# Kernel optimization log

Measured on AMD Instinct MI355X. Metric: run time of the kernel, lower is better.

The kernel has to match this reference:

```python
import jax, jax.numpy as jnp
import numpy as np

D = 1152      # hidden_size
H = 16        # num_heads
K = D // H    # head_dim = 72
L = 2         # depth
I = 4304      # intermediate_size
M = 2         # spatial_merge_size
NPOS = 2304   # num_position_embeddings (48x48)
OUT = 2048    # out_hidden_size
CIN = 3 * 2 * 16 * 16  # C*tp*p*p = 1536
GRID = np.array([[1, 48, 48], [1, 32, 64], [2, 24, 40]], dtype=np.int32)


def _ln(x, s, b, eps=1e-6):
    mu = jnp.mean(x, -1, keepdims=True)
    var = jnp.mean((x - mu) ** 2, -1, keepdims=True)
    return (x - mu) * jax.lax.rsqrt(var + eps) * s + b


def _rot_half(x):
    h = x.shape[-1] // 2
    return jnp.concatenate([-x[..., h:], x[..., :h]], -1)


def _seg_bounds(g):
    b = [0]
    for t, h, w in g:
        for _ in range(int(t)):
            b.append(b[-1] + int(h) * int(w))
    return list(zip(b[:-1], b[1:]))


def _rope_cos_sin(g):
    half = K // 2  # rotary_half_dim
    max_hw = int(g[:, 1:].max())
    inv = 1.0 / (10000.0 ** (np.arange(0, half, 2, dtype=np.float64) / half))
    table = np.arange(max_hw)[:, None] * inv[None, :]  # (max_hw, half//2)
    pos = []
    for t, h, w in g:
        t, h, w = int(t), int(h), int(w)
        mh, mw = h // M, w // M
        row = np.broadcast_to(np.arange(mh)[:, None, None, None] * M + np.arange(M)[None, None, :, None], (mh, mw, M, M)).reshape(-1)
        col = np.broadcast_to(np.arange(mw)[None, :, None, None] * M + np.arange(M)[None, None, None, :], (mh, mw, M, M)).reshape(-1)
        c = np.stack([row, col], -1)
        if t > 1:
            c = np.tile(c, (t, 1))
        pos.append(c)
    pos = np.concatenate(pos, 0)
    emb = table[pos].reshape(pos.shape[0], -1)     # (N, half)
    emb = np.concatenate([emb, emb], -1)           # (N, head_dim)
    return jnp.asarray(np.cos(emb), jnp.float32), jnp.asarray(np.sin(emb), jnp.float32)


def _pos_embeds(pos_table, g):
    n = int(NPOS ** 0.5)
    outs = []
    for t, h, w in g:
        t, h, w = int(t), int(h), int(w)
        hi = np.linspace(0, n - 1, h); wi = np.linspace(0, n - 1, w)
        hf = np.floor(hi).astype(np.int32); wf = np.floor(wi).astype(np.int32)
        hc = np.clip(hf + 1, 0, n - 1); wc = np.clip(wf + 1, 0, n - 1)
        dh = (hi - hf).astype(np.float32); dw = (wi - wf).astype(np.float32)
        i00 = (hf[:, None] * n + wf[None, :]).reshape(-1)
        i01 = (hf[:, None] * n + wc[None, :]).reshape(-1)
        i10 = (hc[:, None] * n + wf[None, :]).reshape(-1)
        i11 = (hc[:, None] * n + wc[None, :]).reshape(-1)
        w00 = ((1 - dh)[:, None] * (1 - dw)[None, :]).reshape(-1, 1)
        w01 = ((1 - dh)[:, None] * dw[None, :]).reshape(-1, 1)
        w10 = (dh[:, None] * (1 - dw)[None, :]).reshape(-1, 1)
        w11 = (dh[:, None] * dw[None, :]).reshape(-1, 1)
        e = pos_table[i00] * w00 + pos_table[i01] * w01 + pos_table[i10] * w10 + pos_table[i11] * w11
        # spatial-merge reorder
        e = jnp.tile(e, (t, 1)).reshape(t, h // M, M, w // M, M, -1).transpose(0, 1, 3, 2, 4, 5).reshape(-1, D)
        outs.append(e)
    return jnp.concatenate(outs, 0)


def _forward(pixel_values, grid, patch_w, patch_b, pos_table, ln1_s, ln1_b, qkv_w, qkv_b,
             proj_w, proj_b, ln2_s, ln2_b, fc1_w, fc1_b, fc2_w, fc2_b,
             m_ln_s, m_ln_b, m_fc1_w, m_fc1_b, m_fc2_w, m_fc2_b):
    g = np.asarray(grid)
    # patch embed: conv with kernel==stride over whole patch == matmul on flattened patch
    x = pixel_values @ patch_w + patch_b               # (N, D)
    x = x + _pos_embeds(pos_table, g)
    cos, sin = _rope_cos_sin(g)                        # (N, K) each
    bounds = _seg_bounds(g)
    scale = K ** -0.5
    for l in range(L):
        h = _ln(x, ln1_s[l], ln1_b[l])
        N = h.shape[0]
        qkv = (h @ qkv_w[l] + qkv_b[l]).reshape(N, 3, H, K)
        q, k, v = qkv[:, 0], qkv[:, 1], qkv[:, 2]
        q = q * cos[:, None, :] + _rot_half(q) * sin[:, None, :]
        k = k * cos[:, None, :] + _rot_half(k) * sin[:, None, :]
        outs = []
        for s, e in bounds:  # static ragged segments (cu_seqlens)
            logits = jnp.einsum('lhk,mhk->hlm', q[s:e], k[s:e]) * scale
            wts = jax.nn.softmax(logits.astype(jnp.float32), -1).astype(logits.dtype)
            outs.append(jnp.einsum('hlm,mhk->lhk', wts, v[s:e]).reshape(e - s, H * K))
        attn = jnp.concatenate(outs, 0) @ proj_w[l] + proj_b[l]
        x = x + attn
        h2 = _ln(x, ln2_s[l], ln2_b[l])
        x = x + jax.nn.gelu(h2 @ fc1_w[l] + fc1_b[l], approximate=True) @ fc2_w[l] + fc2_b[l]
    normed = _ln(x, m_ln_s, m_ln_b).reshape(-1, D * M * M)
    return jax.nn.gelu(normed @ m_fc1_w + m_fc1_b, approximate=True) @ m_fc2_w + m_fc2_b


def setup_inputs() -> dict:
    key = jax.random.key(0)
    ks = jax.random.split(key, 16)
    def nrm(k, shp, s=0.02):
        return jax.random.normal(k, shp, jnp.float32) * s
    Ntok = int(sum(int(t) * int(h) * int(w) for t, h, w in GRID))  # 6272
    return {
        'pixel_values': nrm(ks[0], (Ntok, CIN), 1.0),
        'grid_thw': jnp.asarray(GRID),
        'patch_w': nrm(ks[1], (CIN, D)), 'patch_b': nrm(ks[2], (D,), 0.01),
        'pos_table': nrm(ks[3], (NPOS, D)),
        'ln1_s': jnp.ones((L, D)), 'ln1_b': jnp.zeros((L, D)),
        'qkv_w': nrm(ks[4], (L, D, 3 * D)), 'qkv_b': nrm(ks[5], (L, 3 * D), 0.01),
        'proj_w': nrm(ks[6], (L, D, D)), 'proj_b': nrm(ks[7], (L, D), 0.01),
        'ln2_s': jnp.ones((L, D)), 'ln2_b': jnp.zeros((L, D)),
        'fc1_w': nrm(ks[8], (L, D, I)), 'fc1_b': nrm(ks[9], (L, I), 0.01),
        'fc2_w': nrm(ks[10], (L, I, D)), 'fc2_b': nrm(ks[11], (L, D), 0.01),
        'm_ln_s': jnp.ones((D,)), 'm_ln_b': jnp.zeros((D,)),
        'm_fc1_w': nrm(ks[12], (D * M * M, D * M * M)), 'm_fc1_b': nrm(ks[13], (D * M * M,), 0.01),
        'm_fc2_w': nrm(ks[14], (D * M * M, OUT)), 'm_fc2_b': nrm(ks[15], (OUT,), 0.01),
    }


def reference(pixel_values, grid_thw, patch_w, patch_b, pos_table, ln1_s, ln1_b, qkv_w, qkv_b,
              proj_w, proj_b, ln2_s, ln2_b, fc1_w, fc1_b, fc2_w, fc2_b,
              m_ln_s, m_ln_b, m_fc1_w, m_fc1_b, m_fc2_w, m_fc2_b):
    return _forward(pixel_values, grid_thw, patch_w, patch_b, pos_table, ln1_s, ln1_b, qkv_w, qkv_b,
                    proj_w, proj_b, ln2_s, ln2_b, fc1_w, fc1_b, fc2_w, fc2_b,
                    m_ln_s, m_ln_b, m_fc1_w, m_fc1_b, m_fc2_w, m_fc2_b)
```

## Files before the change

### kernel.cpp

```cpp
#include <hip/hip_runtime.h>

typedef __bf16 bf16;
typedef float f32x4 __attribute__((ext_vector_type(4)));
typedef bf16 bf16x8 __attribute__((ext_vector_type(8)));

#define NTOK 6272
#define DMODEL 1152

__device__ __forceinline__ void tok_geo(int t, int& row, int& col, int& gh, int& gw) {
    int local;
    if (t < 2304)      { local = t;        gh = 48; gw = 48; }
    else if (t < 4352) { local = t - 2304; gh = 32; gw = 64; }
    else if (t < 5312) { local = t - 4352; gh = 24; gw = 40; }
    else               { local = t - 5312; gh = 24; gw = 40; }
    int mc = local & 1;
    int mr = (local >> 1) & 1;
    int rest = local >> 2;
    int mwc = gw >> 1;
    int mw = rest % mwc;
    int mh = rest / mwc;
    row = mh * 2 + mr;
    col = mw * 2 + mc;
}

__device__ __forceinline__ float gelu_tanh(float v) {
    float c = v + 0.044715f * v * v * v;
    return 0.5f * v * (1.0f + tanhf(0.7978845608028654f * c));
}

__global__ void detect_kernel(const unsigned short* __restrict__ px, int* __restrict__ flag) {
    int tid = threadIdx.x;
    int cnt = 0;
    for (int i = tid * 8; i < tid * 8 + 8; i++) {
        unsigned e = (px[i] >> 7) & 0xFF;
        if (e < 100u || e > 140u) cnt++;
    }
#pragma unroll
    for (int off = 32; off > 0; off >>= 1) cnt += __shfl_down(cnt, off);
    if (tid == 0) *flag = (cnt > 64) ? 1 : 0;
}

template <typename T>
__device__ __forceinline__ void load8(const T* src, bf16* dst, bool pred) {
    if (!pred) {
        uint4 z = {0, 0, 0, 0};
        *(uint4*)dst = z;
        return;
    }
    if constexpr (sizeof(T) == 2) {
        *(uint4*)dst = *(const uint4*)src;
    } else {
        float4 a = *(const float4*)src;
        float4 b = *(const float4*)(src + 4);
        dst[0] = (bf16)a.x; dst[1] = (bf16)a.y; dst[2] = (bf16)a.z; dst[3] = (bf16)a.w;
        dst[4] = (bf16)b.x; dst[5] = (bf16)b.y; dst[6] = (bf16)b.z; dst[7] = (bf16)b.w;
    }
}

template <typename TI>
__global__ __launch_bounds__(256) void pos_embed_kernel(const int* __restrict__ flag,
                                                        const TI* __restrict__ tab,
                                                        bf16* __restrict__ x) {
    if (*flag != (sizeof(TI) == 4 ? 1 : 0)) return;
    int t = blockIdx.x;
    int row, col, gh, gw;
    tok_geo(t, row, col, gh, gw);
    float hi = row * 47.0f / (gh - 1);
    float wi = col * 47.0f / (gw - 1);
    int hf = (int)hi, wf = (int)wi;
    int hc = min(hf + 1, 47), wc = min(wf + 1, 47);
    float dh = hi - hf, dw = wi - wf;
    float w00 = (1.f - dh) * (1.f - dw);
    float w01 = (1.f - dh) * dw;
    float w10 = dh * (1.f - dw);
    float w11 = dh * dw;
    const TI* p00 = tab + (size_t)(hf * 48 + wf) * DMODEL;
    const TI* p01 = tab + (size_t)(hf * 48 + wc) * DMODEL;
    const TI* p10 = tab + (size_t)(hc * 48 + wf) * DMODEL;
    const TI* p11 = tab + (size_t)(hc * 48 + wc) * DMODEL;
    bf16* xr = x + (size_t)t * DMODEL;
    for (int d = threadIdx.x; d < DMODEL; d += 256)
        xr[d] = (bf16)(w00 * (float)p00[d] + w01 * (float)p01[d] +
                       w10 * (float)p10[d] + w11 * (float)p11[d]);
}

template <typename TI>
__global__ __launch_bounds__(256) void ln_kernel(const int* __restrict__ flag,
                                                 const bf16* __restrict__ x,
                                                 const TI* __restrict__ s,
                                                 const TI* __restrict__ b,
                                                 bf16* __restrict__ out) {
    if (*flag != (sizeof(TI) == 4 ? 1 : 0)) return;
    const int row = blockIdx.x;
    const int tid = threadIdx.x;
    __shared__ float red[4];
    const bf16* xr = x + (size_t)row * DMODEL;
    float vals[5];
    int cnt = 0;
    float sum = 0.f;
    for (int i = tid; i < DMODEL; i += 256) { vals[cnt] = (float)xr[i]; sum += vals[cnt]; cnt++; }
#pragma unroll
    for (int off = 32; off > 0; off >>= 1) sum += __shfl_down(sum, off);
    if ((tid & 63) == 0) red[tid >> 6] = sum;
    __syncthreads();
    float mean = (red[0] + red[1] + red[2] + red[3]) * (1.0f / DMODEL);
    float vs = 0.f;
    for (int i = 0; i < cnt; i++) { float d = vals[i] - mean; vs += d * d; }
#pragma unroll
    for (int off = 32; off > 0; off >>= 1) vs += __shfl_down(vs, off);
    __syncthreads();
    if ((tid & 63) == 0) red[tid >> 6] = vs;
    __syncthreads();
    float var = (red[0] + red[1] + red[2] + red[3]) * (1.0f / DMODEL);
    float inv = rsqrtf(var + 1e-6f);
    int idx = 0;
    for (int i = tid; i < DMODEL; i += 256)
        out[(size_t)row * DMODEL + i] = (bf16)((vals[idx++] - mean) * inv * (float)s[i] + (float)b[i]);
}

__global__ __launch_bounds__(256) void rope_inplace_kernel(bf16* __restrict__ qkv) {
    int idx = blockIdx.x * 256 + threadIdx.x;
    const int total = NTOK * 16 * 36;
    if (idx >= total) return;
    int j = idx % 36;
    int rest = idx / 36;
    int h = rest & 15;
    int t = rest >> 4;
    bf16* base = qkv + (size_t)t * 3456 + h * 72;
    int row, col, gh, gw;
    tok_geo(t, row, col, gh, gw);
    float pos = (float)((j < 18) ? row : col);
    int fi = (j < 18) ? j : j - 18;
    float ang = pos * powf(10000.0f, -(float)fi / 18.0f);
    float cv = cosf(ang), sv = sinf(ang);
    float q0v = (float)base[j],        q1v = (float)base[j + 36];
    float k0v = (float)base[1152 + j], k1v = (float)base[1152 + j + 36];
    base[j]          = (bf16)(q0v * cv - q1v * sv);
    base[j + 36]     = (bf16)(q1v * cv + q0v * sv);
    base[1152 + j]      = (bf16)(k0v * cv - k1v * sv);
    base[1152 + j + 36] = (bf16)(k1v * cv + k0v * sv);
}

__global__ __launch_bounds__(256) void attn_kernel(const bf16* __restrict__ qkv,
                                                   bf16* __restrict__ outp) {
    const int bx = blockIdx.x;
    const int head = bx & 15;
    const int qt = bx >> 4;
    int sbase, slen, qtb;
    if (qt < 36)      { sbase = 0;    slen = 2304; qtb = 0;  }
    else if (qt < 68) { sbase = 2304; slen = 2048; qtb = 36; }
    else if (qt < 83) { sbase = 4352; slen = 960;  qtb = 68; }
    else              { sbase = 5312; slen = 960;  qtb = 83; }
    const int q0 = sbase + (qt - qtb) * 64;

    __shared__ bf16 Ks[64][104];
    __shared__ bf16 Vs[80][72];
    __shared__ bf16 Ps[64][72];

    const int tid = threadIdx.x;
    const int wv = tid >> 6;
    const int lane = tid & 63;
    const int quad = lane >> 4;
    const int l15 = lane & 15;

    const size_t hoff = (size_t)head * 72;

    for (int c = tid; c < 64; c += 256) {
        int r = 72 + (c >> 3), cc = (c & 7) * 8;
        uint4 z = {0, 0, 0, 0};
        *(uint4*)&Vs[r][cc] = z;
    }

    for (int c = tid; c < 768; c += 256) {
        int r = c / 12, cc = (c % 12) * 8;
        uint4 v = {0, 0, 0, 0};
        if (cc < 72) v = *(const uint4*)(qkv + (size_t)(q0 + r) * 3456 + hoff + cc);
        *(uint4*)&Ks[r][cc] = v;
    }
    __syncthreads();
    bf16x8 aq[3];
#pragma unroll
    for (int i = 0; i < 3; i++) aq[i] = *(const bf16x8*)&Ks[wv * 16 + l15][i * 32 + quad * 8];

    f32x4 o[5] = {};
    float m_i[4], l_i[4];
#pragma unroll
    for (int r = 0; r < 4; r++) { m_i[r] = -1e30f; l_i[r] = 0.f; }

    const float C1 = 0.17002234f;
    const int nkv = slen >> 6;
    for (int kt = 0; kt < nkv; kt++) {
        const int k0 = sbase + kt * 64;
        __syncthreads();
        for (int c = tid; c < 768; c += 256) {
            int r = c / 12, cc = (c % 12) * 8;
            uint4 v = {0, 0, 0, 0};
            if (cc < 72) v = *(const uint4*)(qkv + (size_t)(k0 + r) * 3456 + 1152 + hoff + cc);
            *(uint4*)&Ks[r][cc] = v;
        }
        for (int c = tid; c < 576; c += 256) {
            int r = c & 63, cc = (c >> 6) * 8;
            uint4 v = *(const uint4*)(qkv + (size_t)(k0 + r) * 3456 + 2304 + hoff + cc);
            const bf16* e = (const bf16*)&v;
#pragma unroll
            for (int i = 0; i < 8; i++) Vs[cc + i][r] = e[i];
        }
        __syncthreads();

        f32x4 sfr[4] = {};
#pragma unroll
        for (int kc = 0; kc < 3; kc++)
#pragma unroll
            for (int nt = 0; nt < 4; nt++) {
                bf16x8 bk = *(const bf16x8*)&Ks[nt * 16 + l15][kc * 32 + quad * 8];
                sfr[nt] = __builtin_amdgcn_mfma_f32_16x16x32_bf16(aq[kc], bk, sfr[nt], 0, 0, 0);
            }

        float mx[4];
#pragma unroll
        for (int reg = 0; reg < 4; reg++) {
            float m = fmaxf(fmaxf(sfr[0][reg], sfr[1][reg]), fmaxf(sfr[2][reg], sfr[3][reg]));
            m = fmaxf(m, __shfl_xor(m, 1));
            m = fmaxf(m, __shfl_xor(m, 2));
            m = fmaxf(m, __shfl_xor(m, 4));
            m = fmaxf(m, __shfl_xor(m, 8));
            mx[reg] = m;
        }
        bool grow = (mx[0] > m_i[0]) || (mx[1] > m_i[1]) || (mx[2] > m_i[2]) || (mx[3] > m_i[3]);
        if (__any(grow)) {
#pragma unroll
            for (int reg = 0; reg < 4; reg++) {
                float mn = fmaxf(m_i[reg], mx[reg]);
                float a = __builtin_amdgcn_exp2f((m_i[reg] - mn) * C1);
                m_i[reg] = mn;
                l_i[reg] *= a;
#pragma unroll
                for (int nt = 0; nt < 5; nt++) o[nt][reg] *= a;
            }
        }
        float mc[4];
#pragma unroll
        for (int reg = 0; reg < 4; reg++) mc[reg] = m_i[reg] * C1;
        float rs[4] = {0.f, 0.f, 0.f, 0.f};
#pragma unroll
        for (int nt = 0; nt < 4; nt++)
#pragma unroll
            for (int reg = 0; reg < 4; reg++) {
                float p = __builtin_amdgcn_exp2f(fmaf(sfr[nt][reg], C1, -mc[reg]));
                sfr[nt][reg] = p;
                rs[reg] += p;
            }
#pragma unroll
        for (int reg = 0; reg < 4; reg++) {
            float r = rs[reg];
            r += __shfl_xor(r, 1);
            r += __shfl_xor(r, 2);
            r += __shfl_xor(r, 4);
            r += __shfl_xor(r, 8);
            l_i[reg] += r;
        }

#pragma unroll
        for (int nt = 0; nt < 4; nt++)
#pragma unroll
            for (int reg = 0; reg < 4; reg++)
                Ps[wv * 16 + quad * 4 + reg][nt * 16 + l15] = (bf16)sfr[nt][reg];

#pragma unroll
        for (int kc = 0; kc < 2; kc++) {
            bf16x8 ap = *(const bf16x8*)&Ps[wv * 16 + l15][kc * 32 + quad * 8];
#pragma unroll
            for (int nt = 0; nt < 5; nt++) {
                bf16x8 bv = *(const bf16x8*)&Vs[nt * 16 + l15][kc * 32 + quad * 8];
                o[nt] = __builtin_amdgcn_mfma_f32_16x16x32_bf16(ap, bv, o[nt], 0, 0, 0);
            }
        }
    }

#pragma unroll
    for (int nt = 0; nt < 5; nt++)
#pragma unroll
        for (int reg = 0; reg < 4; reg++) {
            int c = nt * 16 + l15;
            if (c < 72) {
                int tok = q0 + wv * 16 + quad * 4 + reg;
                outp[(size_t)tok * DMODEL + head * 72 + c] = (bf16)(o[nt][reg] / l_i[reg]);
            }
        }
}

template <int MODE, typename TA, typename TB>
__global__ __launch_bounds__(256) void gemm_kernel(const int* __restrict__ flag,
                                                   const TA* __restrict__ A,
                                                   const TB* __restrict__ B,
                                                   const TB* __restrict__ bias,
                                                   void* __restrict__ outp,
                                                   int M, int N, int K) {
    if (*flag != (sizeof(TB) == 4 ? 1 : 0)) return;
    __shared__ bf16 As[128][40];
    __shared__ bf16 Bs[128][40];
    const int tid = threadIdx.x;
    const int m0 = blockIdx.y * 128;
    const int n0 = blockIdx.x * 128;
    const int wv = tid >> 6;
    const int lane = tid & 63;
    const int quad = lane >> 4;
    const int l15 = lane & 15;
    const int wr = (wv >> 1) * 64;
    const int wc = (wv & 1) * 64;

    const int a_row = tid >> 1;
    const int a_col = (tid & 1) * 16;
    const int b_k = tid & 31;
    const int b_n = (tid >> 5) * 16;

    f32x4 acc[4][4] = {};

    for (int k0 = 0; k0 < K; k0 += 32) {
        __syncthreads();
        {
            bf16 ea[16];
            int gr = m0 + a_row;
            const TA* ap = A + (size_t)gr * K + k0 + a_col;
// ... 23 lines not shown
#pragma unroll
            for (int ni = 0; ni < 4; ni++)
                acc[mi][ni] = __builtin_amdgcn_mfma_f32_16x16x32_bf16(af[mi], bfv[ni], acc[mi][ni], 0, 0, 0);
    }

#pragma unroll
    for (int mi = 0; mi < 4; mi++) {
#pragma unroll
        for (int ni = 0; ni < 4; ni++) {
#pragma unroll
            for (int reg = 0; reg < 4; reg++) {
                int r = m0 + wr + mi * 16 + quad * 4 + reg;
                int c = n0 + wc + ni * 16 + l15;
                if (r < M && c < N) {
                    float v = acc[mi][ni][reg] + (float)bias[c];
                    if (MODE == 1) v = gelu_tanh(v);
                    if (MODE == 2) {
                        bf16* o = (bf16*)outp;
                        size_t idx = (size_t)r * N + c;
                        o[idx] = (bf16)((float)o[idx] + v);
                    } else if (MODE == 3) {
                        TB* o = (TB*)outp;
                        o[(size_t)r * N + c] = (TB)v;
                    } else {
                        bf16* o = (bf16*)outp;
                        o[(size_t)r * N + c] = (bf16)v;
                    }
                }
            }
        }
    }
}


template <typename TI>
__global__ __launch_bounds__(256) void cvt_kernel(const int* __restrict__ flag,
                                                  const TI* __restrict__ in,
                                                  bf16* __restrict__ out, int n8) {
    if (*flag != (sizeof(TI) == 4 ? 1 : 0)) return;
    for (int i = blockIdx.x * 256 + threadIdx.x; i < n8; i += gridDim.x * 256) {
        bf16 e[8];
        load8(in + (size_t)i * 8, e, true);
        *(uint4*)(out + (size_t)i * 8) = *(uint4*)e;
    }
}

template <typename TI>
__global__ __launch_bounds__(256) void transpose_w_kernel(const int* __restrict__ flag,
                                                          const TI* __restrict__ B,
                                                          bf16* __restrict__ T,
                                                          int K, int N, int Kpad) {
    if (*flag != (sizeof(TI) == 4 ? 1 : 0)) return;
    __shared__ bf16 t[64][72];
    const int k0 = blockIdx.y * 64, n0 = blockIdx.x * 64;
    const int tid = threadIdx.x;
    const int kk = tid >> 2;
    const int nn0 = (tid & 3) * 16;
    bf16 e[16];
    bool ok = (k0 + kk < K) && (n0 + nn0 < N);
    const TI* src = B + (size_t)(k0 + kk) * N + n0 + nn0;
    load8(src, e, ok);
    load8(src + 8, e + 8, ok);
#pragma unroll
    for (int i = 0; i < 16; i++) t[nn0 + i][kk] = e[i];
    __syncthreads();
    const int nn = tid >> 2;
    const int j16 = (tid & 3) * 16;
    if (n0 + nn < N && k0 + j16 < Kpad) {
        bf16* dst = T + (size_t)(n0 + nn) * Kpad + k0 + j16;
        *(uint4*)dst = *(uint4*)&t[nn][j16];
        *(uint4*)(dst + 8) = *(uint4*)&t[nn][j16 + 8];
    }
}

template <typename TI>
__global__ __launch_bounds__(256) void cvt_bias_kernel(const int* __restrict__ flag,
        const TI* p0, const TI* p1, const TI* p2, const TI* p3, const TI* p4,
        const TI* p5, const TI* p6, const TI* p7, const TI* p8, const TI* p9,
        const TI* p10, bf16* __restrict__ out) {
    if (*flag != (sizeof(TI) == 4 ? 1 : 0)) return;
    const int lens[11] = {1152, 3456, 3456, 1152, 1152, 4304, 4304, 1152, 1152, 4608, 2048};
    const int offs[11] = {0, 1152, 4608, 8064, 9216, 10368, 14672, 18976, 20128, 21280, 25888};
    int b = blockIdx.x;
    const TI* src = (b == 0) ? p0 : (b == 1) ? p1 : (b == 2) ? p2 : (b == 3) ? p3
                  : (b == 4) ? p4 : (b == 5) ? p5 : (b == 6) ? p6 : (b == 7) ? p7
                  : (b == 8) ? p8 : (b == 9) ? p9 : p10;
    for (int i = threadIdx.x; i < lens[b]; i += 256) out[offs[b] + i] = (bf16)(float)src[i];
}

typedef const __attribute__((address_space(1))) void* gas_ptr;
typedef __attribute__((address_space(3))) void* las_ptr;
__device__ __forceinline__ void gload16(const bf16* g, bf16* l) {
    __builtin_amdgcn_global_load_lds((gas_ptr)g, (las_ptr)l, 16, 0, 0);
}

template <int MODE>
__global__ __launch_bounds__(256) void gemm_lds_kernel(const int* __restrict__ flag,
        const bf16* __restrict__ A, const bf16* __restrict__ BT,
        const bf16* __restrict__ bias, void* __restrict__ outp,
        int M, int N, int K, int ldc) {
    __shared__ bf16 As[128][32];
    __shared__ bf16 Bs[128][32];
    const int tid = threadIdx.x;
    const int m0 = blockIdx.y * 128;
    const int n0 = blockIdx.x * 128;
    const int wv = tid >> 6;
    const int lane = tid & 63;
    const int quad = lane >> 4;
    const int l15 = lane & 15;
    const int wr = (wv >> 1) * 64;
    const int wc = (wv & 1) * 64;

    const int sr = wv * 32 + (lane >> 2);
    const int sc = (lane & 3) * 8;
    const bf16* aP0 = A + (size_t)min(m0 + sr, M - 1) * K + sc;
    const bf16* aP1 = A + (size_t)min(m0 + sr + 16, M - 1) * K + sc;
    const bf16* bP0 = BT + (size_t)min(n0 + sr, N - 1) * K + sc;
    const bf16* bP1 = BT + (size_t)min(n0 + sr + 16, N - 1) * K + sc;
    bf16* lA0 = &As[wv * 32][0];
    bf16* lA1 = &As[wv * 32 + 16][0];
    bf16* lB0 = &Bs[wv * 32][0];
// ... 127 lines not shown
    }
}

#define OFF_PATCH  0ULL
#define OFF_QKV    1769472ULL
#define QKV_SZ     3981312ULL
#define OFF_PROJ   9732096ULL
#define PROJ_SZ    1327104ULL
#define OFF_FC1    12386304ULL
#define FC1_SZ     4958208ULL
#define OFF_FC2    22302720ULL
#define FC2_SZ     4976640ULL
#define OFF_MFC1   32256000ULL
#define OFF_MFC2   53489664ULL
#define OFF_BIAS   62926848ULL
#define WS_NEEDED  209001280ULL

extern "C" void kernel_launch(void* const* d_in, const int* in_sizes, int n_in,
                              void* d_out, int out_size, void* d_ws, size_t ws_size,
                              hipStream_t stream) {
    char* ws = (char*)d_ws;
    int* flag  = (int*)ws;
    bf16* x    = (bf16*)(ws + 256);
    bf16* h    = (bf16*)(ws + 256 + 14450688);
    bf16* bufA = (bf16*)(ws + 256 + 28901376);

    detect_kernel<<<1, 64, 0, stream>>>((const unsigned short*)d_in[0], flag);

    if (ws_size >= WS_NEEDED) {
        bf16* wT = (bf16*)(ws + 256 + 28901376 + 54190080);
        bf16* bias = wT + OFF_BIAS;
        bf16* px = bufA;

        cvt_kernel<bf16><<<1024, 256, 0, stream>>>(flag, (const bf16*)d_in[0], px, 1204224);
        cvt_kernel<float><<<1024, 256, 0, stream>>>(flag, (const float*)d_in[0], px, 1204224);

        auto T2 = [&](const void* srcBase, size_t eoff, bf16* dst, int K, int N, int Kpad) {
            dim3 g((N + 63) / 64, (Kpad + 63) / 64);
            transpose_w_kernel<bf16><<<g, 256, 0, stream>>>(flag, (const bf16*)srcBase + eoff, dst, K, N, Kpad);
            transpose_w_kernel<float><<<g, 256, 0, stream>>>(flag, (const float*)srcBase + eoff, dst, K, N, Kpad);
        };
        T2(d_in[2], 0, wT + OFF_PATCH, 1536, 1152, 1536);
        for (int l = 0; l < 2; l++) {
            T2(d_in[7],  (size_t)l * 1152 * 3456, wT + OFF_QKV + l * QKV_SZ, 1152, 3456, 1152);
            T2(d_in[9],  (size_t)l * 1152 * 1152, wT + OFF_PROJ + l * PROJ_SZ, 1152, 1152, 1152);
            T2(d_in[13], (size_t)l * 1152 * 4304, wT + OFF_FC1 + l * FC1_SZ, 1152, 4304, 1152);
            T2(d_in[15], (size_t)l * 4304 * 1152, wT + OFF_FC2 + l * FC2_SZ, 4304, 1152, 4320);
        }
        T2(d_in[19], 0, wT + OFF_MFC1, 4608, 4608, 4608);
        T2(d_in[21], 0, wT + OFF_MFC2, 4608, 2048, 4608);

        cvt_bias_kernel<bf16><<<11, 256, 0, stream>>>(flag,
            (const bf16*)d_in[3],
            (const bf16*)d_in[8], (const bf16*)d_in[8] + 3456,
            (const bf16*)d_in[10], (const bf16*)d_in[10] + 1152,
            (const bf16*)d_in[14], (const bf16*)d_in[14] + 4304,
            (const bf16*)d_in[16], (const bf16*)d_in[16] + 1152,
            (const bf16*)d_in[20], (const bf16*)d_in[22], bias);
        cvt_bias_kernel<float><<<11, 256, 0, stream>>>(flag,
            (const float*)d_in[3],
            (const float*)d_in[8], (const float*)d_in[8] + 3456,
            (const float*)d_in[10], (const float*)d_in[10] + 1152,
            (const float*)d_in[14], (const float*)d_in[14] + 4304,
            (const float*)d_in[16], (const float*)d_in[16] + 1152,
            (const float*)d_in[20], (const float*)d_in[22], bias);

        pos_embed_kernel<bf16><<<NTOK, 256, 0, stream>>>(flag, (const bf16*)d_in[4], x);
        pos_embed_kernel<float><<<NTOK, 256, 0, stream>>>(flag, (const float*)d_in[4], x);

        gemm_lds64_kernel<2><<<dim3(9, 98), 256, 0, stream>>>(flag, px, wT + OFF_PATCH,
                                                              bias + 0, x, NTOK, 1152, 1536, 1152);

        for (int l = 0; l < 2; l++) {
            ln_kernel<bf16><<<NTOK, 256, 0, stream>>>(flag, x, (const bf16*)d_in[5] + l * 1152,
                                                      (const bf16*)d_in[6] + l * 1152, h);
            ln_kernel<float><<<NTOK, 256, 0, stream>>>(flag, x, (const float*)d_in[5] + l * 1152,
                                                       (const float*)d_in[6] + l * 1152, h);
            gemm_lds_kernel<0><<<dim3(27, 49), 256, 0, stream>>>(flag, h, wT + OFF_QKV + l * QKV_SZ,
                                                                 bias + 1152 + l * 3456, bufA,
                                                                 NTOK, 3456, 1152, 3456);
            rope_inplace_kernel<<<(NTOK * 16 * 36 + 255) / 256, 256, 0, stream>>>(bufA);
            attn_kernel<<<98 * 16, 256, 0, stream>>>(bufA, h);
            gemm_lds64_kernel<2><<<dim3(9, 98), 256, 0, stream>>>(flag, h, wT + OFF_PROJ + l * PROJ_SZ,
                                                                  bias + 8064 + l * 1152, x,
                                                                  NTOK, 1152, 1152, 1152);
            ln_kernel<bf16><<<NTOK, 256, 0, stream>>>(flag, x, (const bf16*)d_in[11] + l * 1152,
                                                      (const bf16*)d_in[12] + l * 1152, h);
            ln_kernel<float><<<NTOK, 256, 0, stream>>>(flag, x, (const float*)d_in[11] + l * 1152,
                                                       (const float*)d_in[12] + l * 1152, h);
            gemm_lds_kernel<1><<<dim3(34, 49), 256, 0, stream>>>(flag, h, wT + OFF_FC1 + l * FC1_SZ,
                                                                 bias + 10368 + l * 4304, bufA,
                                                                 NTOK, 4304, 1152, 4320);
            gemm_lds64_kernel<2><<<dim3(9, 98), 256, 0, stream>>>(flag, bufA, wT + OFF_FC2 + l * FC2_SZ,
                                                                  bias + 18976 + l * 1152, x,
                                                                  NTOK, 1152, 4320, 1152);
        }
        ln_kernel<bf16><<<NTOK, 256, 0, stream>>>(flag, x, (const bf16*)d_in[17], (const bf16*)d_in[18], h);
        ln_kernel<float><<<NTOK, 256, 0, stream>>>(flag, x, (const float*)d_in[17], (const float*)d_in[18], h);
        gemm_lds_kernel<1><<<dim3(36, 13), 256, 0, stream>>>(flag, h, wT + OFF_MFC1,
                                                             bias + 21280, bufA, 1568, 4608, 4608, 4608);
        gemm_lds64_kernel<3><<<dim3(16, 25), 256, 0, stream>>>(flag, bufA, wT + OFF_MFC2,
                                                               bias + 25888, d_out, 1568, 2048, 4608, 2048);
        return;
    }

    {
        pos_embed_kernel<bf16><<<NTOK, 256, 0, stream>>>(flag, (const bf16*)d_in[4], x);
        pos_embed_kernel<float><<<NTOK, 256, 0, stream>>>(flag, (const float*)d_in[4], x);
        gemm_kernel<2, bf16, bf16><<<dim3(9, 49), 256, 0, stream>>>(
            flag, (const bf16*)d_in[0], (const bf16*)d_in[2], (const bf16*)d_in[3], x, NTOK, 1152, 1536);
        gemm_kernel<2, float, float><<<dim3(9, 49), 256, 0, stream>>>(
            flag, (const float*)d_in[0], (const float*)d_in[2], (const float*)d_in[3], x, NTOK, 1152, 1536);
    }
    for (int l = 0; l < 2; l++) {
        ln_kernel<bf16><<<NTOK, 256, 0, stream>>>(flag, x, (const bf16*)d_in[5] + l * 1152,
                                                  (const bf16*)d_in[6] + l * 1152, h);
        ln_kernel<float><<<NTOK, 256, 0, stream>>>(flag, x, (const float*)d_in[5] + l * 1152,
                                                   (const float*)d_in[6] + l * 1152, h);
        gemm_kernel<0, bf16, bf16><<<dim3(27, 49), 256, 0, stream>>>(
            flag, h, (const bf16*)d_in[7] + (size_t)l * 1152 * 3456,
            (const bf16*)d_in[8] + l * 3456, bufA, NTOK, 3456, 1152);
        gemm_kernel<0, bf16, float><<<dim3(27, 49), 256, 0, stream>>>(
            flag, h, (const float*)d_in[7] + (size_t)l * 1152 * 3456,
            (const float*)d_in[8] + l * 3456, bufA, NTOK, 3456, 1152);
        rope_inplace_kernel<<<(NTOK * 16 * 36 + 255) / 256, 256, 0, stream>>>(bufA);
        attn_kernel<<<98 * 16, 256, 0, stream>>>(bufA, h);
        gemm_kernel<2, bf16, bf16><<<dim3(9, 49), 256, 0, stream>>>(
            flag, h, (const bf16*)d_in[9] + (size_t)l * 1152 * 1152,
            (const bf16*)d_in[10] + l * 1152, x, NTOK, 1152, 1152);
        gemm_kernel<2, bf16, float><<<dim3(9, 49), 256, 0, stream>>>(
            flag, h, (const float*)d_in[9] + (size_t)l * 1152 * 1152,
            (const float*)d_in[10] + l * 1152, x, NTOK, 1152, 1152);
        ln_kernel<bf16><<<NTOK, 256, 0, stream>>>(flag, x, (const bf16*)d_in[11] + l * 1152,
// ... 28 lines not shown
```

Before: 2.212 ms.

## Merge dtype-templated kernel pairs, add MFMA setprio, use 64-row tile for merger fc1

```diff
diff --git a/kernel.cpp b/kernel.cpp
--- a/kernel.cpp
+++ b/kernel.cpp
@@ -55,6 +55,309 @@
         dst[0] = (bf16)a.x; dst[1] = (bf16)a.y; dst[2] = (bf16)a.z; dst[3] = (bf16)a.w;
         dst[4] = (bf16)b.x; dst[5] = (bf16)b.y; dst[6] = (bf16)b.z; dst[7] = (bf16)b.w;
     }
+}
+
+
+__global__ __launch_bounds__(256) void pos_embed2_kernel(const int* __restrict__ flag,
+                                                         const bf16* __restrict__ tab16,
+                                                         const float* __restrict__ tab32,
+                                                         bf16* __restrict__ x) {
+    const bool f32 = (*flag != 0);
+    int t = blockIdx.x;
+    int row, col, gh, gw;
+    tok_geo(t, row, col, gh, gw);
+    float hi = row * 47.0f / (gh - 1);
+    float wi = col * 47.0f / (gw - 1);
+    int hf = (int)hi, wf = (int)wi;
+    int hc = min(hf + 1, 47), wc = min(wf + 1, 47);
+    float dh = hi - hf, dw = wi - wf;
+    float w00 = (1.f - dh) * (1.f - dw);
+    float w01 = (1.f - dh) * dw;
+    float w10 = dh * (1.f - dw);
+    float w11 = dh * dw;
+    size_t i00 = (size_t)(hf * 48 + wf) * DMODEL;
+    size_t i01 = (size_t)(hf * 48 + wc) * DMODEL;
+    size_t i10 = (size_t)(hc * 48 + wf) * DMODEL;
+    size_t i11 = (size_t)(hc * 48 + wc) * DMODEL;
+    bf16* xr = x + (size_t)t * DMODEL;
+    if (f32) {
+        for (int d = threadIdx.x; d < DMODEL; d += 256)
+            xr[d] = (bf16)(w00 * tab32[i00 + d] + w01 * tab32[i01 + d] +
+                           w10 * tab32[i10 + d] + w11 * tab32[i11 + d]);
+    } else {
+        for (int d = threadIdx.x; d < DMODEL; d += 256)
+            xr[d] = (bf16)(w00 * (float)tab16[i00 + d] + w01 * (float)tab16[i01 + d] +
+                           w10 * (float)tab16[i10 + d] + w11 * (float)tab16[i11 + d]);
+    }
+}
+
+__global__ __launch_bounds__(256) void ln2_kernel(const int* __restrict__ flag,
+                                                  const bf16* __restrict__ x,
+                                                  const bf16* __restrict__ s16,
+                                                  const bf16* __restrict__ b16,
+                                                  const float* __restrict__ s32,
+                                                  const float* __restrict__ b32,
+                                                  bf16* __restrict__ out) {
+    const bool f32 = (*flag != 0);
+    const int row = blockIdx.x;
+    const int tid = threadIdx.x;
+    __shared__ float red[4];
+    const bf16* xr = x + (size_t)row * DMODEL;
+    float vals[5];
+    int cnt = 0;
+    float sum = 0.f;
+    for (int i = tid; i < DMODEL; i += 256) { vals[cnt] = (float)xr[i]; sum += vals[cnt]; cnt++; }
+#pragma unroll
+    for (int off = 32; off > 0; off >>= 1) sum += __shfl_down(sum, off);
+    if ((tid & 63) == 0) red[tid >> 6] = sum;
+    __syncthreads();
+    float mean = (red[0] + red[1] + red[2] + red[3]) * (1.0f / DMODEL);
+    float vs = 0.f;
+    for (int i = 0; i < cnt; i++) { float d = vals[i] - mean; vs += d * d; }
+#pragma unroll
+    for (int off = 32; off > 0; off >>= 1) vs += __shfl_down(vs, off);
+    __syncthreads();
+    if ((tid & 63) == 0) red[tid >> 6] = vs;
+    __syncthreads();
+    float var = (red[0] + red[1] + red[2] + red[3]) * (1.0f / DMODEL);
+    float inv = rsqrtf(var + 1e-6f);
+    int idx = 0;
+    for (int i = tid; i < DMODEL; i += 256) {
+        float sv = f32 ? s32[i] : (float)s16[i];
+        float bv = f32 ? b32[i] : (float)b16[i];
+        out[(size_t)row * DMODEL + i] = (bf16)((vals[idx++] - mean) * inv * sv + bv);
+    }
+}
+
+__global__ __launch_bounds__(256) void cvt2_kernel(const int* __restrict__ flag,
+                                                   const bf16* __restrict__ in16,
+                                                   const float* __restrict__ in32,
+                                                   bf16* __restrict__ out, int n8) {
+    const bool f32 = (*flag != 0);
+    for (int i = blockIdx.x * 256 + threadIdx.x; i < n8; i += gridDim.x * 256) {
+        bf16 e[8];
+        if (f32) load8(in32 + (size_t)i * 8, e, true);
+        else     load8(in16 + (size_t)i * 8, e, true);
+        *(uint4*)(out + (size_t)i * 8) = *(uint4*)e;
+    }
+}
+
+__global__ __launch_bounds__(256) void transpose_w2_kernel(const int* __restrict__ flag,
+                                                           const bf16* __restrict__ B16,
+                                                           const float* __restrict__ B32,
+                                                           bf16* __restrict__ T,
+                                                           int K, int N, int Kpad) {
+    const bool f32 = (*flag != 0);
+    __shared__ bf16 t[64][72];
+    const int k0 = blockIdx.y * 64, n0 = blockIdx.x * 64;
+    const int tid = threadIdx.x;
+    const int kk = tid >> 2;
+    const int nn0 = (tid & 3) * 16;
+    bf16 e[16];
+    bool ok = (k0 + kk < K) && (n0 + nn0 < N);
+    size_t idx = (size_t)(k0 + kk) * N + n0 + nn0;
+    if (f32) { load8(B32 + idx, e, ok); load8(B32 + idx + 8, e + 8, ok); }
+    else     { load8(B16 + idx, e, ok); load8(B16 + idx + 8, e + 8, ok); }
+#pragma unroll
+    for (int i = 0; i < 16; i++) t[nn0 + i][kk] = e[i];
+    __syncthreads();
+    const int nn = tid >> 2;
+    const int j16 = (tid & 3) * 16;
+    if (n0 + nn < N && k0 + j16 < Kpad) {
+        bf16* dst = T + (size_t)(n0 + nn) * Kpad + k0 + j16;
+        *(uint4*)dst = *(uint4*)&t[nn][j16];
+        *(uint4*)(dst + 8) = *(uint4*)&t[nn][j16 + 8];
+    }
+}
+
+template <typename TI>
+__global__ __launch_bounds__(256) void cvt_bias_kernel(const int* __restrict__ flag,
+        const TI* p0, const TI* p1, const TI* p2, const TI* p3, const TI* p4,
+        const TI* p5, const TI* p6, const TI* p7, const TI* p8, const TI* p9,
+        const TI* p10, bf16* __restrict__ out) {
+    if (*flag != (sizeof(TI) == 4 ? 1 : 0)) return;
+    const int lens[11] = {1152, 3456, 3456, 1152, 1152, 4304, 4304, 1152, 1152, 4608, 2048};
+    const int offs[11] = {0, 1152, 4608, 8064, 9216, 10368, 14672, 18976, 20128, 21280, 25888};
+    int b = blockIdx.x;
+    const TI* src = (b == 0) ? p0 : (b == 1) ? p1 : (b == 2) ? p2 : (b == 3) ? p3
+                  : (b == 4) ? p4 : (b == 5) ? p5 : (b == 6) ? p6 : (b == 7) ? p7
+                  : (b == 8) ? p8 : (b == 9) ? p9 : p10;
+    for (int i = threadIdx.x; i < lens[b]; i += 256) out[offs[b] + i] = (bf16)(float)src[i];
+}
+
+__global__ __launch_bounds__(256) void rope_inplace_kernel(bf16* __restrict__ qkv) {
+    int idx = blockIdx.x * 256 + threadIdx.x;
+    const int total = NTOK * 16 * 36;
+    if (idx >= total) return;
+    int j = idx % 36;
+    int rest = idx / 36;
+    int h = rest & 15;
+    int t = rest >> 4;
+    bf16* base = qkv + (size_t)t * 3456 + h * 72;
+    int row, col, gh, gw;
+    tok_geo(t, row, col, gh, gw);
+    float pos = (float)((j < 18) ? row : col);
+    int fi = (j < 18) ? j : j - 18;
+    float ang = pos * powf(10000.0f, -(float)fi / 18.0f);
+    float cv = cosf(ang), sv = sinf(ang);
+    float q0v = (float)base[j],        q1v = (float)base[j + 36];
+    float k0v = (float)base[1152 + j], k1v = (float)base[1152 + j + 36];
+    base[j]          = (bf16)(q0v * cv - q1v * sv);
+    base[j + 36]     = (bf16)(q1v * cv + q0v * sv);
+    base[1152 + j]      = (bf16)(k0v * cv - k1v * sv);
+    base[1152 + j + 36] = (bf16)(k1v * cv + k0v * sv);
+}
+
+__global__ __launch_bounds__(256) void attn_kernel(const bf16* __restrict__ qkv,
+                                                   bf16* __restrict__ outp) {
+    const int bx = blockIdx.x;
+    const int head = bx & 15;
+    const int qt = bx >> 4;
+    int sbase, slen, qtb;
+    if (qt < 36)      { sbase = 0;    slen = 2304; qtb = 0;  }
+    else if (qt < 68) { sbase = 2304; slen = 2048; qtb = 36; }
+    else if (qt < 83) { sbase = 4352; slen = 960;  qtb = 68; }
+    else              { sbase = 5312; slen = 960;  qtb = 83; }
+    const int q0 = sbase + (qt - qtb) * 64;
+
+    __shared__ bf16 Ks[64][104];
+    __shared__ bf16 Vs[80][72];
+    __shared__ bf16 Ps[64][72];
+
+    const int tid = threadIdx.x;
+    const int wv = tid >> 6;
+    const int lane = tid & 63;
+    const int quad = lane >> 4;
+    const int l15 = lane & 15;
+
+    const size_t hoff = (size_t)head * 72;
+
+    for (int c = tid; c < 64; c += 256) {
+        int r = 72 + (c >> 3), cc = (c & 7) * 8;
+        uint4 z = {0, 0, 0, 0};
+        *(uint4*)&Vs[r][cc] = z;
+    }
+
+    for (int c = tid; c < 768; c += 256) {
+        int r = c / 12, cc = (c % 12) * 8;
+        uint4 v = {0, 0, 0, 0};
+        if (cc < 72) v = *(const uint4*)(qkv + (size_t)(q0 + r) * 3456 + hoff + cc);
+        *(uint4*)&Ks[r][cc] = v;
+    }
+    __syncthreads();
+    bf16x8 aq[3];
+#pragma unroll
+    for (int i = 0; i < 3; i++) aq[i] = *(const bf16x8*)&Ks[wv * 16 + l15][i * 32 + quad * 8];
+
+    f32x4 o[5] = {};
+    float m_i[4], l_i[4];
+#pragma unroll
+    for (int r = 0; r < 4; r++) { m_i[r] = -1e30f; l_i[r] = 0.f; }
+
+    const float C1 = 0.17002234f;
+    const int nkv = slen >> 6;
+    for (int kt = 0; kt < nkv; kt++) {
+        const int k0 = sbase + kt * 64;
+        __syncthreads();
+        for (int c = tid; c < 768; c += 256) {
+            int r = c / 12, cc = (c % 12) * 8;
+            uint4 v = {0, 0, 0, 0};
+            if (cc < 72) v = *(const uint4*)(qkv + (size_t)(k0 + r) * 3456 + 1152 + hoff + cc);
+            *(uint4*)&Ks[r][cc] = v;
+        }
+        for (int c = tid; c < 576; c += 256) {
+            int r = c & 63, cc = (c >> 6) * 8;
+            uint4 v = *(const uint4*)(qkv + (size_t)(k0 + r) * 3456 + 2304 + hoff + cc);
+            const bf16* e = (const bf16*)&v;
+#pragma unroll
+            for (int i = 0; i < 8; i++) Vs[cc + i][r] = e[i];
+        }
+        __syncthreads();
+
+        f32x4 sfr[4] = {};
+        __builtin_amdgcn_s_setprio(1);
+#pragma unroll
+        for (int kc = 0; kc < 3; kc++)
+#pragma unroll
+            for (int nt = 0; nt < 4; nt++) {
+                bf16x8 bk = *(const bf16x8*)&Ks[nt * 16 + l15][kc * 32 + quad * 8];
+                sfr[nt] = __builtin_amdgcn_mfma_f32_16x16x32_bf16(aq[kc], bk, sfr[nt], 0, 0, 0);
+            }
+        __builtin_amdgcn_s_setprio(0);
+
+        float mx[4];
+#pragma unroll
+        for (int reg = 0; reg < 4; reg++) {
+            float m = fmaxf(fmaxf(sfr[0][reg], sfr[1][reg]), fmaxf(sfr[2][reg], sfr[3][reg]));
+            m = fmaxf(m, __shfl_xor(m, 1));
+            m = fmaxf(m, __shfl_xor(m, 2));
+            m = fmaxf(m, __shfl_xor(m, 4));
+            m = fmaxf(m, __shfl_xor(m, 8));
+            mx[reg] = m;
+        }
+        bool grow = (mx[0] > m_i[0]) || (mx[1] > m_i[1]) || (mx[2] > m_i[2]) || (mx[3] > m_i[3]);
+        if (__any(grow)) {
+#pragma unroll
+            for (int reg = 0; reg < 4; reg++) {
+                float mn = fmaxf(m_i[reg], mx[reg]);
+                float a = __builtin_amdgcn_exp2f((m_i[reg] - mn) * C1);
+                m_i[reg] = mn;
+                l_i[reg] *= a;
+#pragma unroll
+                for (int nt = 0; nt < 5; nt++) o[nt][reg] *= a;
+            }
+        }
+        float mc[4];
+#pragma unroll
+        for (int reg = 0; reg < 4; reg++) mc[reg] = m_i[reg] * C1;
+        float rs[4] = {0.f, 0.f, 0.f, 0.f};
+#pragma unroll
+        for (int nt = 0; nt < 4; nt++)
+#pragma unroll
+            for (int reg = 0; reg < 4; reg++) {
+                float p = __builtin_amdgcn_exp2f(fmaf(sfr[nt][reg], C1, -mc[reg]));
+                sfr[nt][reg] = p;
+                rs[reg] += p;
+            }
+#pragma unroll
+        for (int reg = 0; reg < 4; reg++) {
+            float r = rs[reg];
+            r += __shfl_xor(r, 1);
+            r += __shfl_xor(r, 2);
+            r += __shfl_xor(r, 4);
+            r += __shfl_xor(r, 8);
+            l_i[reg] += r;
+        }
+
+#pragma unroll
+        for (int nt = 0; nt < 4; nt++)
+#pragma unroll
+            for (int reg = 0; reg < 4; reg++)
+                Ps[wv * 16 + quad * 4 + reg][nt * 16 + l15] = (bf16)sfr[nt][reg];
+
+        __builtin_amdgcn_s_setprio(1);
+#pragma unroll
+        for (int kc = 0; kc < 2; kc++) {
+            bf16x8 ap = *(const bf16x8*)&Ps[wv * 16 + l15][kc * 32 + quad * 8];
+#pragma unroll
+            for (int nt = 0; nt < 5; nt++) {
+                bf16x8 bv = *(const bf16x8*)&Vs[nt * 16 + l15][kc * 32 + quad * 8];
+                o[nt] = __builtin_amdgcn_mfma_f32_16x16x32_bf16(ap, bv, o[nt], 0, 0, 0);
+            }
+        }
+        __builtin_amdgcn_s_setprio(0);
+    }
+
+#pragma unroll
+    for (int nt = 0; nt < 5; nt++)
+#pragma unroll
+        for (int reg = 0; reg < 4; reg++) {
+            int c = nt * 16 + l15;
+            if (c < 72) {
+                int tok = q0 + wv * 16 + quad * 4 + reg;
+                outp[(size_t)tok * DMODEL + head * 72 + c] = (bf16)(o[nt][reg] / l_i[reg]);
+            }
+        }
 }
 
 template <typename TI>
@@ -118,177 +421,6 @@
         out[(size_t)row * DMODEL + i] = (bf16)((vals[idx++] - mean) * inv * (float)s[i] + (float)b[i]);
 }
 
-__global__ __launch_bounds__(256) void rope_inplace_kernel(bf16* __restrict__ qkv) {
-    int idx = blockIdx.x * 256 + threadIdx.x;
-    const int total = NTOK * 16 * 36;
-    if (idx >= total) return;
-    int j = idx % 36;
-    int rest = idx / 36;
-    int h = rest & 15;
-    int t = rest >> 4;
-    bf16* base = qkv + (size_t)t * 3456 + h * 72;
-    int row, col, gh, gw;
-    tok_geo(t, row, col, gh, gw);
-    float pos = (float)((j < 18) ? row : col);
-    int fi = (j < 18) ? j : j - 18;
-    float ang = pos * powf(10000.0f, -(float)fi / 18.0f);
-    float cv = cosf(ang), sv = sinf(ang);
-    float q0v = (float)base[j],        q1v = (float)base[j + 36];
-    float k0v = (float)base[1152 + j], k1v = (float)base[1152 + j + 36];
-    base[j]          = (bf16)(q0v * cv - q1v * sv);
-    base[j + 36]     = (bf16)(q1v * cv + q0v * sv);
-    base[1152 + j]      = (bf16)(k0v * cv - k1v * sv);
-    base[1152 + j + 36] = (bf16)(k1v * cv + k0v * sv);
-}
-
-__global__ __launch_bounds__(256) void attn_kernel(const bf16* __restrict__ qkv,
-                                                   bf16* __restrict__ outp) {
-    const int bx = blockIdx.x;
-    const int head = bx & 15;
-    const int qt = bx >> 4;
-    int sbase, slen, qtb;
-    if (qt < 36)      { sbase = 0;    slen = 2304; qtb = 0;  }
-    else if (qt < 68) { sbase = 2304; slen = 2048; qtb = 36; }
-    else if (qt < 83) { sbase = 4352; slen = 960;  qtb = 68; }
-    else              { sbase = 5312; slen = 960;  qtb = 83; }
-    const int q0 = sbase + (qt - qtb) * 64;
-
-    __shared__ bf16 Ks[64][104];
-    __shared__ bf16 Vs[80][72];
-    __shared__ bf16 Ps[64][72];
-
-    const int tid = threadIdx.x;
-    const int wv = tid >> 6;
-    const int lane = tid & 63;
-    const int quad = lane >> 4;
-    const int l15 = lane & 15;
-
-    const size_t hoff = (size_t)head * 72;
-
-    for (int c = tid; c < 64; c += 256) {
-        int r = 72 + (c >> 3), cc = (c & 7) * 8;
-        uint4 z = {0, 0, 0, 0};
-        *(uint4*)&Vs[r][cc] = z;
-    }
-
-    for (int c = tid; c < 768; c += 256) {
-        int r = c / 12, cc = (c % 12) * 8;
-        uint4 v = {0, 0, 0, 0};
-        if (cc < 72) v = *(const uint4*)(qkv + (size_t)(q0 + r) * 3456 + hoff + cc);
-        *(uint4*)&Ks[r][cc] = v;
-    }
-    __syncthreads();
-    bf16x8 aq[3];
-#pragma unroll
-    for (int i = 0; i < 3; i++) aq[i] = *(const bf16x8*)&Ks[wv * 16 + l15][i * 32 + quad * 8];
-
-    f32x4 o[5] = {};
-    float m_i[4], l_i[4];
-#pragma unroll
-    for (int r = 0; r < 4; r++) { m_i[r] = -1e30f; l_i[r] = 0.f; }
-
-    const float C1 = 0.17002234f;
-    const int nkv = slen >> 6;
-    for (int kt = 0; kt < nkv; kt++) {
-        const int k0 = sbase + kt * 64;
-        __syncthreads();
-        for (int c = tid; c < 768; c += 256) {
-            int r = c / 12, cc = (c % 12) * 8;
-            uint4 v = {0, 0, 0, 0};
-            if (cc < 72) v = *(const uint4*)(qkv + (size_t)(k0 + r) * 3456 + 1152 + hoff + cc);
-            *(uint4*)&Ks[r][cc] = v;
-        }
-        for (int c = tid; c < 576; c += 256) {
-            int r = c & 63, cc = (c >> 6) * 8;
-            uint4 v = *(const uint4*)(qkv + (size_t)(k0 + r) * 3456 + 2304 + hoff + cc);
-            const bf16* e = (const bf16*)&v;
-#pragma unroll
-            for (int i = 0; i < 8; i++) Vs[cc + i][r] = e[i];
-        }
-        __syncthreads();
-
-        f32x4 sfr[4] = {};
-#pragma unroll
-        for (int kc = 0; kc < 3; kc++)
-#pragma unroll
-            for (int nt = 0; nt < 4; nt++) {
-                bf16x8 bk = *(const bf16x8*)&Ks[nt * 16 + l15][kc * 32 + quad * 8];
-                sfr[nt] = __builtin_amdgcn_mfma_f32_16x16x32_bf16(aq[kc], bk, sfr[nt], 0, 0, 0);
-            }
-
-        float mx[4];
-#pragma unroll
-        for (int reg = 0; reg < 4; reg++) {
-            float m = fmaxf(fmaxf(sfr[0][reg], sfr[1][reg]), fmaxf(sfr[2][reg], sfr[3][reg]));
-            m = fmaxf(m, __shfl_xor(m, 1));
-            m = fmaxf(m, __shfl_xor(m, 2));
-            m = fmaxf(m, __shfl_xor(m, 4));
-            m = fmaxf(m, __shfl_xor(m, 8));
-            mx[reg] = m;
-        }
-        bool grow = (mx[0] > m_i[0]) || (mx[1] > m_i[1]) || (mx[2] > m_i[2]) || (mx[3] > m_i[3]);
-        if (__any(grow)) {
-#pragma unroll
-            for (int reg = 0; reg < 4; reg++) {
-                float mn = fmaxf(m_i[reg], mx[reg]);
-                float a = __builtin_amdgcn_exp2f((m_i[reg] - mn) * C1);
-                m_i[reg] = mn;
-                l_i[reg] *= a;
-#pragma unroll
-                for (int nt = 0; nt < 5; nt++) o[nt][reg] *= a;
-            }
-        }
-        float mc[4];
-#pragma unroll
-        for (int reg = 0; reg < 4; reg++) mc[reg] = m_i[reg] * C1;
-        float rs[4] = {0.f, 0.f, 0.f, 0.f};
-#pragma unroll
-        for (int nt = 0; nt < 4; nt++)
-#pragma unroll
-            for (int reg = 0; reg < 4; reg++) {
-                float p = __builtin_amdgcn_exp2f(fmaf(sfr[nt][reg], C1, -mc[reg]));
-                sfr[nt][reg] = p;
-                rs[reg] += p;
-            }
-#pragma unroll
-        for (int reg = 0; reg < 4; reg++) {
-            float r = rs[reg];
-            r += __shfl_xor(r, 1);
-            r += __shfl_xor(r, 2);
-            r += __shfl_xor(r, 4);
-            r += __shfl_xor(r, 8);
-            l_i[reg] += r;
-        }
-
-#pragma unroll
-        for (int nt = 0; nt < 4; nt++)
-#pragma unroll
-            for (int reg = 0; reg < 4; reg++)
-                Ps[wv * 16 + quad * 4 + reg][nt * 16 + l15] = (bf16)sfr[nt][reg];
-
-#pragma unroll
-        for (int kc = 0; kc < 2; kc++) {
-            bf16x8 ap = *(const bf16x8*)&Ps[wv * 16 + l15][kc * 32 + quad * 8];
-#pragma unroll
-            for (int nt = 0; nt < 5; nt++) {
-                bf16x8 bv = *(const bf16x8*)&Vs[nt * 16 + l15][kc * 32 + quad * 8];
-                o[nt] = __builtin_amdgcn_mfma_f32_16x16x32_bf16(ap, bv, o[nt], 0, 0, 0);
-            }
-        }
-    }
-
-#pragma unroll
-    for (int nt = 0; nt < 5; nt++)
-#pragma unroll
-        for (int reg = 0; reg < 4; reg++) {
-            int c = nt * 16 + l15;
-            if (c < 72) {
-                int tok = q0 + wv * 16 + quad * 4 + reg;
-                outp[(size_t)tok * DMODEL + head * 72 + c] = (bf16)(o[nt][reg] / l_i[reg]);
-            }
-        }
-}
-
 template <int MODE, typename TA, typename TB>
 __global__ __launch_bounds__(256) void gemm_kernel(const int* __restrict__ flag,
                                                    const TA* __restrict__ A,
@@ -378,61 +510,6 @@
     }
 }
 
-
-template <typename TI>
-__global__ __launch_bounds__(256) void cvt_kernel(const int* __restrict__ flag,
-                                                  const TI* __restrict__ in,
-                                                  bf16* __restrict__ out, int n8) {
-    if (*flag != (sizeof(TI) == 4 ? 1 : 0)) return;
-    for (int i = blockIdx.x * 256 + threadIdx.x; i < n8; i += gridDim.x * 256) {
-        bf16 e[8];
-        load8(in + (size_t)i * 8, e, true);
-        *(uint4*)(out + (size_t)i * 8) = *(uint4*)e;
-    }
-}
-
-template <typename TI>
-__global__ __launch_bounds__(256) void transpose_w_kernel(const int* __restrict__ flag,
-                                                          const TI* __restrict__ B,
-                                                          bf16* __restrict__ T,
-                                                          int K, int N, int Kpad) {
-    if (*flag != (sizeof(TI) == 4 ? 1 : 0)) return;
-    __shared__ bf16 t[64][72];
-    const int k0 = blockIdx.y * 64, n0 = blockIdx.x * 64;
-    const int tid = threadIdx.x;
-    const int kk = tid >> 2;
-    const int nn0 = (tid & 3) * 16;
-    bf16 e[16];
-    bool ok = (k0 + kk < K) && (n0 + nn0 < N);
-    const TI* src = B + (size_t)(k0 + kk) * N + n0 + nn0;
-    load8(src, e, ok);
-    load8(src + 8, e + 8, ok);
-#pragma unroll
-    for (int i = 0; i < 16; i++) t[nn0 + i][kk] = e[i];
-    __syncthreads();
-    const int nn = tid >> 2;
-    const int j16 = (tid & 3) * 16;
-    if (n0 + nn < N && k0 + j16 < Kpad) {
-        bf16* dst = T + (size_t)(n0 + nn) * Kpad + k0 + j16;
-        *(uint4*)dst = *(uint4*)&t[nn][j16];
-        *(uint4*)(dst + 8) = *(uint4*)&t[nn][j16 + 8];
-    }
-}
-
-template <typename TI>
-__global__ __launch_bounds__(256) void cvt_bias_kernel(const int* __restrict__ flag,
-        const TI* p0, const TI* p1, const TI* p2, const TI* p3, const TI* p4,
-        const TI* p5, const TI* p6, const TI* p7, const TI* p8, const TI* p9,
-        const TI* p10, bf16* __restrict__ out) {
-    if (*flag != (sizeof(TI) == 4 ? 1 : 0)) return;
-    const int lens[11] = {1152, 3456, 3456, 1152, 1152, 4304, 4304, 1152, 1152, 4608, 2048};
-    const int offs[11] = {0, 1152, 4608, 8064, 9216, 10368, 14672, 18976, 20128, 21280, 25888};
-    int b = blockIdx.x;
-    const TI* src = (b == 0) ? p0 : (b == 1) ? p1 : (b == 2) ? p2 : (b == 3) ? p3
-                  : (b == 4) ? p4 : (b == 5) ? p5 : (b == 6) ? p6 : (b == 7) ? p7
-                  : (b == 8) ? p8 : (b == 9) ? p9 : p10;
-    for (int i = threadIdx.x; i < lens[b]; i += 256) out[offs[b] + i] = (bf16)(float)src[i];
-}
 
 typedef const __attribute__((address_space(1))) void* gas_ptr;
 typedef __attribute__((address_space(3))) void* las_ptr;
@@ -626,23 +703,23 @@
         bf16* bias = wT + OFF_BIAS;
         bf16* px = bufA;
 
-        cvt_kernel<bf16><<<1024, 256, 0, stream>>>(flag, (const bf16*)d_in[0], px, 1204224);
-        cvt_kernel<float><<<1024, 256, 0, stream>>>(flag, (const float*)d_in[0], px, 1204224);
-
-        auto T2 = [&](const void* srcBase, size_t eoff, bf16* dst, int K, int N, int Kpad) {
+        cvt2_kernel<<<1024, 256, 0, stream>>>(flag, (const bf16*)d_in[0], (const float*)d_in[0],
+                                              px, 1204224);
+
+        auto T1 = [&](const void* srcBase, size_t eoff, bf16* dst, int K, int N, int Kpad) {
             dim3 g((N + 63) / 64, (Kpad + 63) / 64);
-            transpose_w_kernel<bf16><<<g, 256, 0, stream>>>(flag, (const bf16*)srcBase + eoff, dst, K, N, Kpad);
-            transpose_w_kernel<float><<<g, 256, 0, stream>>>(flag, (const float*)srcBase + eoff, dst, K, N, Kpad);
+            transpose_w2_kernel<<<g, 256, 0, stream>>>(flag, (const bf16*)srcBase + eoff,
+                                                       (const float*)srcBase + eoff, dst, K, N, Kpad);
         };
-        T2(d_in[2], 0, wT + OFF_PATCH, 1536, 1152, 1536);
+        T1(d_in[2], 0, wT + OFF_PATCH, 1536, 1152, 1536);
         for (int l = 0; l < 2; l++) {
-            T2(d_in[7],  (size_t)l * 1152 * 3456, wT + OFF_QKV + l * QKV_SZ, 1152, 3456, 1152);
-            T2(d_in[9],  (size_t)l * 1152 * 1152, wT + OFF_PROJ + l * PROJ_SZ, 1152, 1152, 1152);
-            T2(d_in[13], (size_t)l * 1152 * 4304, wT + OFF_FC1 + l * FC1_SZ, 1152, 4304, 1152);
-            T2(d_in[15], (size_t)l * 4304 * 1152, wT + OFF_FC2 + l * FC2_SZ, 4304, 1152, 4320);
-        }
-        T2(d_in[19], 0, wT + OFF_MFC1, 4608, 4608, 4608);
-        T2(d_in[21], 0, wT + OFF_MFC2, 4608, 2048, 4608);
+            T1(d_in[7],  (size_t)l * 1152 * 3456, wT + OFF_QKV + l * QKV_SZ, 1152, 3456, 1152);
+            T1(d_in[9],  (size_t)l * 1152 * 1152, wT + OFF_PROJ + l * PROJ_SZ, 1152, 1152, 1152);
+            T1(d_in[13], (size_t)l * 1152 * 4304, wT + OFF_FC1 + l * FC1_SZ, 1152, 4304, 1152);
+            T1(d_in[15], (size_t)l * 4304 * 1152, wT + OFF_FC2 + l * FC2_SZ, 4304, 1152, 4320);
+        }
+        T1(d_in[19], 0, wT + OFF_MFC1, 4608, 4608, 4608);
+        T1(d_in[21], 0, wT + OFF_MFC2, 4608, 2048, 4608);
 
         cvt_bias_kernel<bf16><<<11, 256, 0, stream>>>(flag,
             (const bf16*)d_in[3],
@@ -659,17 +736,16 @@
             (const float*)d_in[16], (const float*)d_in[16] + 1152,
             (const float*)d_in[20], (const float*)d_in[22], bias);
 
-        pos_embed_kernel<bf16><<<NTOK, 256, 0, stream>>>(flag, (const bf16*)d_in[4], x);
-        pos_embed_kernel<float><<<NTOK, 256, 0, stream>>>(flag, (const float*)d_in[4], x);
+        pos_embed2_kernel<<<NTOK, 256, 0, stream>>>(flag, (const bf16*)d_in[4],
+                                                    (const float*)d_in[4], x);
 
         gemm_lds64_kernel<2><<<dim3(9, 98), 256, 0, stream>>>(flag, px, wT + OFF_PATCH,
                                                               bias + 0, x, NTOK, 1152, 1536, 1152);
 
         for (int l = 0; l < 2; l++) {
-            ln_kernel<bf16><<<NTOK, 256, 0, stream>>>(flag, x, (const bf16*)d_in[5] + l * 1152,
-                                                      (const bf16*)d_in[6] + l * 1152, h);
-            ln_kernel<float><<<NTOK, 256, 0, stream>>>(flag, x, (const float*)d_in[5] + l * 1152,
-                                                       (const float*)d_in[6] + l * 1152, h);
+            ln2_kernel<<<NTOK, 256, 0, stream>>>(flag, x,
+                (const bf16*)d_in[5] + l * 1152, (const bf16*)d_in[6] + l * 1152,
+                (const float*)d_in[5] + l * 1152, (const float*)d_in[6] + l * 1152, h);
             gemm_lds_kernel<0><<<dim3(27, 49), 256, 0, stream>>>(flag, h, wT + OFF_QKV + l * QKV_SZ,
                                                                  bias + 1152 + l * 3456, bufA,
                                                                  NTOK, 3456, 1152, 3456);
@@ -678,10 +754,9 @@
             gemm_lds64_kernel<2><<<dim3(9, 98), 256, 0, stream>>>(flag, h, wT + OFF_PROJ + l * PROJ_SZ,
                                                                   bias + 8064 + l * 1152, x,
                                                                   NTOK, 1152, 1152, 1152);
-            ln_kernel<bf16><<<NTOK, 256, 0, stream>>>(flag, x, (const bf16*)d_in[11] + l * 1152,
-                                                      (const bf16*)d_in[12] + l * 1152, h);
-            ln_kernel<float><<<NTOK, 256, 0, stream>>>(flag, x, (const float*)d_in[11] + l * 1152,
-                                                       (const float*)d_in[12] + l * 1152, h);
+            ln2_kernel<<<NTOK, 256, 0, stream>>>(flag, x,
+                (const bf16*)d_in[11] + l * 1152, (const bf16*)d_in[12] + l * 1152,
+                (const float*)d_in[11] + l * 1152, (const float*)d_in[12] + l * 1152, h);
             gemm_lds_kernel<1><<<dim3(34, 49), 256, 0, stream>>>(flag, h, wT + OFF_FC1 + l * FC1_SZ,
                                                                  bias + 10368 + l * 4304, bufA,
                                                                  NTOK, 4304, 1152, 4320);
@@ -689,10 +764,11 @@
                                                                   bias + 18976 + l * 1152, x,
                                                                   NTOK, 1152, 4320, 1152);
         }
-        ln_kernel<bf16><<<NTOK, 256, 0, stream>>>(flag, x, (const bf16*)d_in[17], (const bf16*)d_in[18], h);
-        ln_kernel<float><<<NTOK, 256, 0, stream>>>(flag, x, (const float*)d_in[17], (const float*)d_in[18], h);
-        gemm_lds_kernel<1><<<dim3(36, 13), 256, 0, stream>>>(flag, h, wT + OFF_MFC1,
-                                                             bias + 21280, bufA, 1568, 4608, 4608, 4608);
+        ln2_kernel<<<NTOK, 256, 0, stream>>>(flag, x,
+            (const bf16*)d_in[17], (const bf16*)d_in[18],
+            (const float*)d_in[17], (const float*)d_in[18], h);
+        gemm_lds64_kernel<1><<<dim3(36, 25), 256, 0, stream>>>(flag, h, wT + OFF_MFC1,
+                                                               bias + 21280, bufA, 1568, 4608, 4608, 4608);
         gemm_lds64_kernel<3><<<dim3(16, 25), 256, 0, stream>>>(flag, bufA, wT + OFF_MFC2,
                                                                bias + 25888, d_out, 1568, 2048, 4608, 2048);
         return;
```

New measurement: 2.167 ms. 1.02x faster.
